# Kernel optimization log

Measured on AMD Instinct MI355X. Metric: run time of the kernel, lower is better.

## Reference

```python
import jax, jax.numpy as jnp
import numpy as np

C = 256          # channels
KS = 7           # kernel_size
G = 256          # groups (defaults to channels)
HID = C // 4     # hidden = channels // reduction
BN_EPS = 1e-5


def setup_inputs() -> dict:
    key = jax.random.key(0)
    ks = jax.random.split(key, 4)
    B, H, W = 4, 64, 64
    return {
        "x": jax.random.normal(ks[0], (B, C, H, W), jnp.float32),
        "reduce_w": jax.random.normal(ks[1], (HID, C), jnp.float32) / np.float32(np.sqrt(C)),
        "bn_gamma": jnp.ones((HID,), jnp.float32),
        "bn_beta": jnp.zeros((HID,), jnp.float32),
        "bn_mean": jnp.zeros((HID,), jnp.float32),
        "bn_var": jnp.ones((HID,), jnp.float32),
        "kproj_w": jax.random.normal(ks[2], (KS * KS * G, HID), jnp.float32) / np.float32(np.sqrt(HID)),
        "kproj_b": jnp.zeros((KS * KS * G,), jnp.float32),
    }


def _kernels(x, reduce_w, bn_gamma, bn_beta, bn_mean, bn_var, kproj_w, kproj_b):
    # 1x1 conv -> BN (eval mode) -> ReLU -> 1x1 conv, then per-pixel L2 kernel norm
    B, _, H, W = x.shape
    h = jnp.einsum('bchw,oc->bohw', x, reduce_w)
    inv = bn_gamma / jnp.sqrt(bn_var + BN_EPS)
    h = h * inv[None, :, None, None] + (bn_beta - bn_mean * inv)[None, :, None, None]
    h = jax.nn.relu(h)
    ker = jnp.einsum('bchw,oc->bohw', h, kproj_w) + kproj_b[None, :, None, None]
    ker = ker.reshape(B, G, KS * KS, H, W)           # (B, G, k*k, H, W)
    # kernel_norm == 'l2': zero-mean + unit L2 norm over the k*k taps
    ker = ker - ker.mean(axis=2, keepdims=True)
    denom = jnp.maximum(jnp.sqrt(jnp.sum(ker * ker, axis=2, keepdims=True)), 1e-6)
    return ker / denom


def reference(x, reduce_w, bn_gamma, bn_beta, bn_mean, bn_var, kproj_w, kproj_b):
    # get_kernels is under @torch.no_grad() in the original -> stop_gradient
    ker = jax.lax.stop_gradient(
        _kernels(x, reduce_w, bn_gamma, bn_beta, bn_mean, bn_var, kproj_w, kproj_b))
    B, Cc, H, W = x.shape
    pad = KS // 2
    gc = Cc // G  # = 1 for depthwise involution
    xp = jnp.pad(x, ((0, 0), (0, 0), (pad, pad), (pad, pad)))
    xg = xp.reshape(B, G, gc, H + 2 * pad, W + 2 * pad)
    # fused unfold-multiply-accumulate over the k*k taps (no (B,C,k,k,H,W) tensor)
    out = jnp.zeros((B, G, gc, H, W), x.dtype)
    for t in range(KS * KS):
        i, j = divmod(t, KS)
        out = out + xg[:, :, :, i:i + H, j:j + W] * ker[:, :, t][:, :, None]
    return out.reshape(B, Cc, H, W)
```

## Files before the change

### kernel.cpp

```cpp
#include <hip/hip_runtime.h>


#define C_    256
#define HID_  64
#define KS_   7
#define KK_   49
#define G_    256
#define H_    64
#define W_    64
#define HW_   4096
#define BN_EPS 1e-5f

typedef __attribute__((ext_vector_type(8)))  short bf16x8;
typedef __attribute__((ext_vector_type(4)))  float f32x4;
typedef __attribute__((ext_vector_type(16))) float f32x16;
typedef __attribute__((ext_vector_type(2)))  unsigned uv2;

__device__ __forceinline__ ushort f2bf(float f) {
    unsigned u = __float_as_uint(f);
    return (ushort)((u + 0x7fffu + ((u >> 16) & 1u)) >> 16);
}
__device__ __forceinline__ float bf2f(ushort s) {
    return __uint_as_float((unsigned)s << 16);
}
__device__ __forceinline__ float xor32p(float v) {
#if __has_builtin(__builtin_amdgcn_permlane32_swap)
    uv2 r = __builtin_amdgcn_permlane32_swap(__float_as_uint(v), __float_as_uint(v),
                                             false, false);
    return (__uint_as_float(r[0]) + __uint_as_float(r[1])) - v;
#else
    return __shfl_xor(v, 32);
#endif
}

__global__ __launch_bounds__(256) void prep_kernel(
    const float* __restrict__ kw, const float* __restrict__ kb,
    const float* __restrict__ reduce_w,
    const float* __restrict__ bn_gamma, const float* __restrict__ bn_beta,
    const float* __restrict__ bn_mean, const float* __restrict__ bn_var,
    ushort* __restrict__ kwb, float* __restrict__ rwT, float* __restrict__ betp,
    float* __restrict__ kbp)
{
    const int bid = blockIdx.x;
    if (bid < 256) {
        int idx  = bid * 256 + threadIdx.x;
        int base = idx * 16;
        int g    = base >> 12;
        int rem  = base & 4095;
        int tp   = rem >> 6;
        int k0   = rem & 63;
        if (tp >= 56) return;
        union { ushort s[16]; uint4 v[2]; } u;
        if ((tp & 7) < 7) {
            int t = (tp >> 3) * 7 + (tp & 7);
            const float* src = kw + ((size_t)(g * KK_ + t)) * HID_ + k0;
            #pragma unroll
            for (int i = 0; i < 16; ++i) u.s[i] = f2bf(src[i]);
        } else {
            #pragma unroll
            for (int i = 0; i < 16; ++i) u.s[i] = 0;
        }
        uint4* dst = (uint4*)(kwb + base);
        dst[0] = u.v[0];
        dst[1] = u.v[1];
    } else if (bid == 256) {
        int k = threadIdx.x;
        #pragma unroll 1
        for (int o = 0; o < HID_; ++o) {
            float inv = bn_gamma[o] * rsqrtf(bn_var[o] + BN_EPS);
            rwT[k * HID_ + o] = reduce_w[o * C_ + k] * inv;
        }
        if (k < HID_) {
            float inv = bn_gamma[k] * rsqrtf(bn_var[k] + BN_EPS);
            betp[k] = bn_beta[k] - bn_mean[k] * inv;
        }
    } else if (bid == 257) {
        for (int i = threadIdx.x; i < G_ * 64; i += 256) {
            int g = i >> 6, tp = i & 63;
            if (tp >= 56) continue;
            kbp[i] = ((tp & 7) < 7) ? kb[g * KK_ + (tp >> 3) * 7 + (tp & 7)] : 0.f;
        }
    } else {
        const int g = bid - 258;
        __shared__ float part[4][64];
        const int k  = threadIdx.x & 63;
        const int pr = threadIdx.x >> 6;
        const int t0 = pr * 13;
        const int t1 = (t0 + 13 < KK_) ? t0 + 13 : KK_;
        float s = 0.f;
        for (int t = t0; t < t1; ++t)
            s += kw[((size_t)(g * KK_ + t)) * HID_ + k];
        part[pr][k] = s;
        __syncthreads();
        if (threadIdx.x < 64) {
            float u = part[0][k] + part[1][k] + part[2][k] + part[3][k];
            ushort uh = f2bf(u);
            ushort ul = f2bf(u - bf2f(uh));
            ushort* kg = kwb + (size_t)g * 4096;
            kg[56 * 64 + k] = uh;  kg[60 * 64 + k] = uh;
            kg[57 * 64 + k] = ul;  kg[61 * 64 + k] = ul;
            kg[58 * 64 + k] = 0;   kg[59 * 64 + k] = 0;
            kg[62 * 64 + k] = 0;   kg[63 * 64 + k] = 0;
            float bs = (k < KK_) ? kb[g * KK_ + k] : 0.f;
            #pragma unroll
            for (int off = 32; off >= 1; off >>= 1) bs += __shfl_xor(bs, off);
            if (k == 0) {
                float* bg = kbp + g * 64;
                bg[56] = bs; bg[60] = bs;
                bg[57] = 0.f; bg[58] = 0.f; bg[59] = 0.f;
                bg[61] = 0.f; bg[62] = 0.f; bg[63] = 0.f;
            }
        }
    }
}

__global__ __launch_bounds__(256) void hv1_kernel(
    const float* __restrict__ x, const float* __restrict__ rwT,
    float* __restrict__ hvp, int npx)
{
    const int lane = threadIdx.x & 63;
    const int wq   = __builtin_amdgcn_readfirstlane(threadIdx.x >> 6);
    const int kq   = blockIdx.y;
    const int p    = blockIdx.x * 64 + lane;
    const int b    = p >> 12;
    const int hw   = p & 4095;

    float acc[16];
    #pragma unroll
    for (int j = 0; j < 16; ++j) acc[j] = 0.f;

    const float* xp = x + ((size_t)b * C_ + kq * 64) * HW_ + hw;
    const float* rw = rwT + (kq * 64) * HID_ + wq * 16;
    #pragma unroll 8
    for (int kk = 0; kk < 64; ++kk) {
        float xk = xp[(size_t)kk * HW_];
        #pragma unroll
        for (int j = 0; j < 16; ++j) acc[j] = fmaf(xk, rw[kk * HID_ + j], acc[j]);
    }
    float* dst = hvp + ((size_t)(kq * 64 + wq * 16)) * npx + p;
    #pragma unroll
    for (int j = 0; j < 16; ++j) dst[(size_t)j * npx] = acc[j];
}

__global__ __launch_bounds__(256) void hv2_kernel(
    const float* __restrict__ hvp, const float* __restrict__ betp,
    ushort* __restrict__ hv, int npx)
{
    const int p  = blockIdx.x * 256 + threadIdx.x;
    const int o0 = blockIdx.y * 4;
    ushort s[4];
    #pragma unroll
    for (int j = 0; j < 4; ++j) {
        float v = 0.f;
        #pragma unroll
        for (int kq = 0; kq < 4; ++kq)
            v += hvp[(size_t)(kq * 64 + o0 + j) * npx + p];
        s[j] = f2bf(fmaxf(v + betp[o0 + j], 0.f));
    }
    uint2 w;
    w.x = (uint)s[0] | ((uint)s[1] << 16);
    w.y = (uint)s[2] | ((uint)s[3] << 16);
    *(uint2*)(hv + (size_t)p * HID_ + o0) = w;
}

__global__ __launch_bounds__(256) void hv_kernel(
    const float* __restrict__ x, const float* __restrict__ rwT,
    const float* __restrict__ betp, ushort* __restrict__ hv)
{
    const int lane = threadIdx.x & 63;
    const int q    = __builtin_amdgcn_readfirstlane(threadIdx.x >> 6);
    const int p    = blockIdx.x * 64 + lane;
    const int b    = p >> 12;
    const int hw   = p & 4095;
    float acc[16];
    #pragma unroll
    for (int j = 0; j < 16; ++j) acc[j] = betp[q * 16 + j];
    const float* xp = x + (size_t)b * C_ * HW_ + hw;
    #pragma unroll 8
    for (int k = 0; k < C_; ++k) {
        float xk = xp[(size_t)k * HW_];
        const float* rw = rwT + k * HID_ + q * 16;
        #pragma unroll
        for (int j = 0; j < 16; ++j) acc[j] = fmaf(xk, rw[j], acc[j]);
    }
    union { ushort s[16]; uint4 v[2]; } u;
    #pragma unroll
    for (int j = 0; j < 16; ++j) u.s[j] = f2bf(fmaxf(acc[j], 0.f));
    uint4* dst = (uint4*)(hv + (size_t)p * HID_ + q * 16);
    dst[0] = u.v[0];
    dst[1] = u.v[1];
}

__global__ __launch_bounds__(64) void invol_main(
    const float* __restrict__ x, const ushort* __restrict__ hv,
    const ushort* __restrict__ kwb, const float* __restrict__ kbp,
    float* __restrict__ out)
{
    __shared__ float x_s[22][72];
    __shared__ float hs_s[22][64];

    const int lane = threadIdx.x;
    const int bg   = blockIdx.x;
    const int b    = bg >> 8;
    const int g    = bg & 255;
    const int y0   = blockIdx.y << 4;
    const int l31  = lane & 31;
    const int h4   = (lane >> 5) * 4;
    const int kl16 = (lane >> 5) * 16;
    const int c0   = h4 + l31;

    const float* xg = x + (size_t)bg * HW_;
    for (int idx = lane; idx < 22 * 72; idx += 64) {
        int r = idx / 72, c = idx - r * 72;
        int yy = y0 - 3 + r;
        int cc = c - 3;
        bool v = ((unsigned)yy < 64u) && ((unsigned)cc < 64u);
        x_s[r][c] = v ? xg[yy * 64 + cc] : 0.f;
    }

    bf16x8 ka[2][4];
    const char* kwg = (const char*)kwb + (size_t)g * 8192;
    #pragma unroll
    for (int m = 0; m < 2; ++m)
        #pragma unroll
        for (int s = 0; s < 4; ++s)
            ka[m][s] = *(const bf16x8*)(kwg + (m * 32 + l31) * 128 + s * 32 + kl16);
    const float* kbg = kbp + g * 64 + h4;

    __syncthreads();

    for (int t = lane; t < 88; t += 64) {
        int r   = t >> 2;
        int cc0 = (t & 3) << 4;
        float v[22];
        #pragma unroll
        for (int i = 0; i < 22; ++i) v[i] = x_s[r][cc0 + i];
        float s = v[0] + v[1] + v[2] + v[3] + v[4] + v[5] + v[6];
        hs_s[r][cc0] = s;
        #pragma unroll
        for (int c = 1; c < 16; ++c) {
            s += v[c + 6] - v[c - 1];
            hs_s[r][cc0 + c] = s;
        }
    }
    __syncthreads();

    const int rowpix0 = (b << 12) + (y0 << 6);

    #pragma unroll 2
    for (int ry = 0; ry < 16; ++ry) {
        bf16x8 hb0[4], hb1[4];
        const char* hvrow = (const char*)hv + (size_t)(rowpix0 + (ry << 6)) * 128;
        #pragma unroll
        for (int s = 0; s < 4; ++s) {
            hb0[s] = *(const bf16x8*)(hvrow + l31 * 128 + s * 32 + kl16);
            hb1[s] = *(const bf16x8*)(hvrow + (32 + l31) * 128 + s * 32 + kl16);
        }
        f32x4 kv0[4], kv1[4];
        #pragma unroll
        for (int q = 0; q < 4; ++q) {
            kv0[q] = *(const f32x4*)(kbg + q * 8);
            kv1[q] = *(const f32x4*)(kbg + 32 + q * 8);
        }

        float x2 = hs_s[ry][lane] + hs_s[ry + 1][lane] + hs_s[ry + 2][lane]
                 + hs_s[ry + 3][lane] + hs_s[ry + 4][lane]
                 + hs_s[ry + 5][lane] + hs_s[ry + 6][lane];

        f32x16 acc00, acc01, acc10, acc11;
        #pragma unroll
        for (int q = 0; q < 4; ++q)
            #pragma unroll
            for (int e = 0; e < 4; ++e) {
                acc00[q * 4 + e] = kv0[q][e];
                acc01[q * 4 + e] = kv0[q][e];
                acc10[q * 4 + e] = kv1[q][e];
                acc11[q * 4 + e] = kv1[q][e];
            }
        #pragma unroll
        for (int s = 0; s < 4; ++s) {
            acc00 = __builtin_amdgcn_mfma_f32_32x32x16_bf16(ka[0][s], hb0[s], acc00, 0, 0, 0);
            acc01 = __builtin_amdgcn_mfma_f32_32x32x16_bf16(ka[0][s], hb1[s], acc01, 0, 0, 0);
            acc10 = __builtin_amdgcn_mfma_f32_32x32x16_bf16(ka[1][s], hb0[s], acc10, 0, 0, 0);
            acc11 = __builtin_amdgcn_mfma_f32_32x32x16_bf16(ka[1][s], hb1[s], acc11, 0, 0, 0);
        }

        float ssq0 = 0.f, ssq1 = 0.f;
        #pragma unroll
        for (int r = 0; r < 16; ++r) {
            ssq0 = fmaf(acc00[r], acc00[r], ssq0);
            ssq1 = fmaf(acc01[r], acc01[r], ssq1);
        }
        #pragma unroll
        for (int r = 0; r < 12; ++r) {
            ssq0 = fmaf(acc10[r], acc10[r], ssq0);
            ssq1 = fmaf(acc11[r], acc11[r], ssq1);
        }
        float mn0 = (acc10[12] + acc10[13]) * (1.f / 49.f);
        float mn1 = (acc11[12] + acc11[13]) * (1.f / 49.f);

        float kx0 = 0.f, kx1 = 0.f;
        const float* xb = &x_s[ry][0];
        #pragma unroll
        for (int q = 0; q < 4; ++q) {
            const float* bp = xb + q * 72 + c0;
            #pragma unroll
            for (int e = 0; e < 4; ++e) {
                kx0 = fmaf(acc00[q * 4 + e], bp[e], kx0);
                kx1 = fmaf(acc01[q * 4 + e], bp[32 + e], kx1);
            }
        }
        #pragma unroll
        for (int q = 0; q < 3; ++q) {
            const float* bp = xb + (4 + q) * 72 + c0;
            #pragma unroll
            for (int e = 0; e < 4; ++e) {
                kx0 = fmaf(acc10[q * 4 + e], bp[e], kx0);
                kx1 = fmaf(acc11[q * 4 + e], bp[32 + e], kx1);
            }
        }

        const bool lo = lane < 32;
        float kx_own = lo ? kx0 : kx1, kx_cr = lo ? kx1 : kx0;
        float ss_own = lo ? ssq0 : ssq1, ss_cr = lo ? ssq1 : ssq0;
        float mo     = lo ? mn0 : mn1;
        float kxo = kx_own + xor32p(kx_cr);
        float sso = ss_own + xor32p(ss_cr);

        float ss = fmaxf(sso - 49.f * mo * mo, 0.f);
        float is = 1.f / fmaxf(sqrtf(ss), 1e-6f);
        out[(size_t)bg * HW_ + ((y0 + ry) << 6) + lane] = (kxo - mo * x2) * is;
    }
}

__global__ __launch_bounds__(256) void invol_fallback(
    const float* __restrict__ x, const float* __restrict__ reduce_w,
    const float* __restrict__ bn_gamma, const float* __restrict__ bn_beta,
    const float* __restrict__ bn_mean, const float* __restrict__ bn_var,
    const float* __restrict__ kw, const float* __restrict__ kb,
    float* __restrict__ out)
{
    __shared__ float rwT[C_][HID_ + 4];
    __shared__ float bns[HID_];
    __shared__ float bnb[HID_];
    const int tid = threadIdx.x;
    const int b  = blockIdx.z;
    const int g0 = blockIdx.y * 32;
    const int p  = blockIdx.x * 256 + tid;
    const int py = p >> 6;
    const int px = p & 63;
    #pragma unroll 1
    for (int o = 0; o < HID_; ++o) rwT[tid][o] = reduce_w[o * C_ + tid];
    if (tid < HID_) {
        float inv = bn_gamma[tid] * rsqrtf(bn_var[tid] + BN_EPS);
        bns[tid] = inv;
        bnb[tid] = bn_beta[tid] - bn_mean[tid] * inv;
    }
    __syncthreads();
    float hvv[HID_];
    #pragma unroll
    for (int o = 0; o < HID_; ++o) hvv[o] = 0.f;
    const float* xb = x + (size_t)b * C_ * HW_ + p;
    #pragma unroll 4
    for (int k = 0; k < C_; ++k) {
        float xk = xb[(size_t)k * HW_];
        const float4* wr = (const float4*)&rwT[k][0];
        #pragma unroll
        for (int o4 = 0; o4 < HID_ / 4; ++o4) {
            float4 w = wr[o4];
            hvv[o4*4+0] = fmaf(xk, w.x, hvv[o4*4+0]);
            hvv[o4*4+1] = fmaf(xk, w.y, hvv[o4*4+1]);
            hvv[o4*4+2] = fmaf(xk, w.z, hvv[o4*4+2]);
            hvv[o4*4+3] = fmaf(xk, w.w, hvv[o4*4+3]);
        }
    }
    #pragma unroll
    for (int o = 0; o < HID_; ++o) hvv[o] = fmaxf(fmaf(hvv[o], bns[o], bnb[o]), 0.f);
    #pragma unroll 1
    for (int gi = 0; gi < 32; ++gi) {
        const int g = g0 + gi;
        const float* kwg = kw + (size_t)g * KK_ * HID_;
        float acc[KK_];
        #pragma unroll
        for (int t = 0; t < KK_; ++t) {
            float a = kb[g * KK_ + t];
            const float4* row = (const float4*)(kwg + t * HID_);
            #pragma unroll
            for (int k4 = 0; k4 < HID_ / 4; ++k4) {
                float4 w = row[k4];
                a = fmaf(w.x, hvv[k4*4+0], a);
                a = fmaf(w.y, hvv[k4*4+1], a);
                a = fmaf(w.z, hvv[k4*4+2], a);
                a = fmaf(w.w, hvv[k4*4+3], a);
            }
            acc[t] = a;
        }
        float mean = 0.f;
        #pragma unroll
        for (int t = 0; t < KK_; ++t) mean += acc[t];
        mean *= (1.f / 49.f);
        float ss = 0.f;
        #pragma unroll
        for (int t = 0; t < KK_; ++t) { acc[t] -= mean; ss = fmaf(acc[t], acc[t], ss); }
        float inv = 1.f / fmaxf(sqrtf(ss), 1e-6f);
        const float* xg = x + ((size_t)(b * G_ + g)) * HW_;
        float oacc = 0.f;
        #pragma unroll
        for (int i = 0; i < KS_; ++i) {
            int yv = py + i - 3;
            bool rok = ((unsigned)yv < (unsigned)H_);
            const float* xrow = xg + yv * W_;
            #pragma unroll
            for (int j = 0; j < KS_; ++j) {
                int xx = px + j - 3;
                bool ok = rok && ((unsigned)xx < (unsigned)W_);
                float v = ok ? xrow[xx] : 0.f;
                oacc = fmaf(v, acc[i*7+j], oacc);
            }
        }
        out[((size_t)(b * G_ + g)) * HW_ + p] = oacc * inv;
    }
}

extern "C" void kernel_launch(void* const* d_in, const int* in_sizes, int n_in,
                              void* d_out, int out_size, void* d_ws, size_t ws_size,
                              hipStream_t stream) {
    const float* x        = (const float*)d_in[0];
    const float* reduce_w = (const float*)d_in[1];
    const float* bn_gamma = (const float*)d_in[2];
    const float* bn_beta  = (const float*)d_in[3];
    const float* bn_mean  = (const float*)d_in[4];
    const float* bn_var   = (const float*)d_in[5];
    const float* kproj_w  = (const float*)d_in[6];
    const float* kproj_b  = (const float*)d_in[7];
    float* out = (float*)d_out;
    const int B   = in_sizes[0] / (C_ * HW_);
    const int npx = B * HW_;

    size_t kwb_off = 0;
    size_t kwb_sz  = (size_t)G_ * 64 * 64 * 2;
    size_t kbp_off = kwb_off + kwb_sz;
    size_t kbp_sz  = (size_t)G_ * 64 * 4;
    size_t rwt_off = kbp_off + kbp_sz;
    size_t rwt_sz  = (size_t)C_ * HID_ * 4;
    size_t bet_off = rwt_off + rwt_sz;
    size_t bet_sz  = 256;
    size_t hv_off  = bet_off + bet_sz;
    size_t hv_sz   = (size_t)npx * HID_ * 2;
    size_t hvp_off = hv_off + hv_sz;
    size_t hvp_sz  = (size_t)4 * HID_ * npx * 4;
    size_t need2   = hvp_off;
    size_t need    = hvp_off + hvp_sz;

    if (ws_size < need2) {
        dim3 grid(HW_ / 256, G_ / 32, B);
        invol_fallback<<<grid, 256, 0, stream>>>(x, reduce_w, bn_gamma, bn_beta,
                                                 bn_mean, bn_var, kproj_w, kproj_b, out);
        return;
    }

    ushort* kwb  = (ushort*)((char*)d_ws + kwb_off);
    float*  kbp  = (float*)((char*)d_ws + kbp_off);
    float*  rwT  = (float*)((char*)d_ws + rwt_off);
    float*  betp = (float*)((char*)d_ws + bet_off);
    ushort* hv   = (ushort*)((char*)d_ws + hv_off);
    float*  hvp  = (float*)((char*)d_ws + hvp_off);

    prep_kernel<<<dim3(258 + G_), 256, 0, stream>>>(kproj_w, kproj_b, reduce_w,
                                                    bn_gamma, bn_beta, bn_mean, bn_var,
                                                    kwb, rwT, betp, kbp);
    if (ws_size >= need) {
        hv1_kernel<<<dim3(npx / 64, 4), 256, 0, stream>>>(x, rwT, hvp, npx);
        hv2_kernel<<<dim3(npx / 256, 16), 256, 0, stream>>>(hvp, betp, hv, npx);
    } else {
        hv_kernel<<<dim3(npx / 64), 256, 0, stream>>>(x, rwT, betp, hv);
    }
    invol_main<<<dim3(B * G_, 4), 64, 0, stream>>>(x, hv, kwb, kbp, out);
}
```

Before: 124.8 us.

## Halve row tile per block, split MFMA halves sequentially, slide vertical box sum

Each invol_main block now covers 8 output rows instead of 16, so the grid doubles to 8 blocks per (batch, group). The per-row work processes the two 32-pixel halves one after another with two accumulators instead of four, which lowers register pressure and should raise occupancy. The vertical 7-row box sum x2 is now updated incrementally instead of recomputed every row. In exchange, the halo rows of x and the kernel weight loads are repeated across twice as many blocks, and the extra xor shuffles per half add some cost.

```diff
diff --git a/kernel.cpp b/kernel.cpp
--- a/kernel.cpp
+++ b/kernel.cpp
@@ -196,21 +196,21 @@
     const ushort* __restrict__ kwb, const float* __restrict__ kbp,
     float* __restrict__ out)
 {
-    __shared__ float x_s[22][72];
-    __shared__ float hs_s[22][64];
+    __shared__ float x_s[14][72];
+    __shared__ float hs_s[14][64];
 
     const int lane = threadIdx.x;
     const int bg   = blockIdx.x;
     const int b    = bg >> 8;
     const int g    = bg & 255;
-    const int y0   = blockIdx.y << 4;
+    const int y0   = blockIdx.y << 3;
     const int l31  = lane & 31;
     const int h4   = (lane >> 5) * 4;
     const int kl16 = (lane >> 5) * 16;
     const int c0   = h4 + l31;
 
     const float* xg = x + (size_t)bg * HW_;
-    for (int idx = lane; idx < 22 * 72; idx += 64) {
+    for (int idx = lane; idx < 14 * 72; idx += 64) {
         int r = idx / 72, c = idx - r * 72;
         int yy = y0 - 3 + r;
         int cc = c - 3;
@@ -229,9 +229,9 @@
 
     __syncthreads();
 
-    for (int t = lane; t < 88; t += 64) {
-        int r   = t >> 2;
-        int cc0 = (t & 3) << 4;
+    if (lane < 56) {
+        int r   = lane >> 2;
+        int cc0 = (lane & 3) << 4;
         float v[22];
         #pragma unroll
         for (int i = 0; i < 22; ++i) v[i] = x_s[r][cc0 + i];
@@ -247,89 +247,75 @@
 
     const int rowpix0 = (b << 12) + (y0 << 6);
 
+    float x2 = hs_s[0][lane] + hs_s[1][lane] + hs_s[2][lane] + hs_s[3][lane]
+             + hs_s[4][lane] + hs_s[5][lane] + hs_s[6][lane];
+
     #pragma unroll 2
-    for (int ry = 0; ry < 16; ++ry) {
-        bf16x8 hb0[4], hb1[4];
+    for (int ry = 0; ry < 8; ++ry) {
         const char* hvrow = (const char*)hv + (size_t)(rowpix0 + (ry << 6)) * 128;
-        #pragma unroll
-        for (int s = 0; s < 4; ++s) {
-            hb0[s] = *(const bf16x8*)(hvrow + l31 * 128 + s * 32 + kl16);
-            hb1[s] = *(const bf16x8*)(hvrow + (32 + l31) * 128 + s * 32 + kl16);
-        }
         f32x4 kv0[4], kv1[4];
         #pragma unroll
         for (int q = 0; q < 4; ++q) {
             kv0[q] = *(const f32x4*)(kbg + q * 8);
             kv1[q] = *(const f32x4*)(kbg + 32 + q * 8);
         }
-
-        float x2 = hs_s[ry][lane] + hs_s[ry + 1][lane] + hs_s[ry + 2][lane]
-                 + hs_s[ry + 3][lane] + hs_s[ry + 4][lane]
-                 + hs_s[ry + 5][lane] + hs_s[ry + 6][lane];
-
-        f32x16 acc00, acc01, acc10, acc11;
-        #pragma unroll
-        for (int q = 0; q < 4; ++q)
-            #pragma unroll
-            for (int e = 0; e < 4; ++e) {
-                acc00[q * 4 + e] = kv0[q][e];
-                acc01[q * 4 + e] = kv0[q][e];
-                acc10[q * 4 + e] = kv1[q][e];
-                acc11[q * 4 + e] = kv1[q][e];
-            }
-        #pragma unroll
-        for (int s = 0; s < 4; ++s) {
-            acc00 = __builtin_amdgcn_mfma_f32_32x32x16_bf16(ka[0][s], hb0[s], acc00, 0, 0, 0);
-            acc01 = __builtin_amdgcn_mfma_f32_32x32x16_bf16(ka[0][s], hb1[s], acc01, 0, 0, 0);
-            acc10 = __builtin_amdgcn_mfma_f32_32x32x16_bf16(ka[1][s], hb0[s], acc10, 0, 0, 0);
-            acc11 = __builtin_amdgcn_mfma_f32_32x32x16_bf16(ka[1][s], hb1[s], acc11, 0, 0, 0);
-        }
-
-        float ssq0 = 0.f, ssq1 = 0.f;
-        #pragma unroll
-        for (int r = 0; r < 16; ++r) {
-            ssq0 = fmaf(acc00[r], acc00[r], ssq0);
-            ssq1 = fmaf(acc01[r], acc01[r], ssq1);
-        }
-        #pragma unroll
-        for (int r = 0; r < 12; ++r) {
-            ssq0 = fmaf(acc10[r], acc10[r], ssq0);
-            ssq1 = fmaf(acc11[r], acc11[r], ssq1);
-        }
-        float mn0 = (acc10[12] + acc10[13]) * (1.f / 49.f);
-        float mn1 = (acc11[12] + acc11[13]) * (1.f / 49.f);
-
-        float kx0 = 0.f, kx1 = 0.f;
         const float* xb = &x_s[ry][0];
-        #pragma unroll
-        for (int q = 0; q < 4; ++q) {
-            const float* bp = xb + q * 72 + c0;
-            #pragma unroll
-            for (int e = 0; e < 4; ++e) {
-                kx0 = fmaf(acc00[q * 4 + e], bp[e], kx0);
-                kx1 = fmaf(acc01[q * 4 + e], bp[32 + e], kx1);
-            }
-        }
-        #pragma unroll
-        for (int q = 0; q < 3; ++q) {
-            const float* bp = xb + (4 + q) * 72 + c0;
-            #pragma unroll
-            for (int e = 0; e < 4; ++e) {
-                kx0 = fmaf(acc10[q * 4 + e], bp[e], kx0);
-                kx1 = fmaf(acc11[q * 4 + e], bp[32 + e], kx1);
-            }
-        }
-
-        const bool lo = lane < 32;
-        float kx_own = lo ? kx0 : kx1, kx_cr = lo ? kx1 : kx0;
-        float ss_own = lo ? ssq0 : ssq1, ss_cr = lo ? ssq1 : ssq0;
-        float mo     = lo ? mn0 : mn1;
-        float kxo = kx_own + xor32p(kx_cr);
-        float sso = ss_own + xor32p(ss_cr);
-
-        float ss = fmaxf(sso - 49.f * mo * mo, 0.f);
-        float is = 1.f / fmaxf(sqrtf(ss), 1e-6f);
-        out[(size_t)bg * HW_ + ((y0 + ry) << 6) + lane] = (kxo - mo * x2) * is;
+
+        float ov[2];
+        #pragma unroll
+        for (int nh = 0; nh < 2; ++nh) {
+            bf16x8 hb[4];
+            #pragma unroll
+            for (int s = 0; s < 4; ++s)
+                hb[s] = *(const bf16x8*)(hvrow + (nh * 32 + l31) * 128 + s * 32 + kl16);
+
+            f32x16 acc0, acc1;
+            #pragma unroll
+            for (int q = 0; q < 4; ++q)
+                #pragma unroll
+                for (int e = 0; e < 4; ++e) {
+                    acc0[q * 4 + e] = kv0[q][e];
+                    acc1[q * 4 + e] = kv1[q][e];
+                }
+            #pragma unroll
+            for (int s = 0; s < 4; ++s) {
+                acc0 = __builtin_amdgcn_mfma_f32_32x32x16_bf16(ka[0][s], hb[s], acc0, 0, 0, 0);
+                acc1 = __builtin_amdgcn_mfma_f32_32x32x16_bf16(ka[1][s], hb[s], acc1, 0, 0, 0);
+            }
+
+            float ssq = 0.f;
+            #pragma unroll
+            for (int r = 0; r < 16; ++r) ssq = fmaf(acc0[r], acc0[r], ssq);
+            #pragma unroll
+            for (int r = 0; r < 12; ++r) ssq = fmaf(acc1[r], acc1[r], ssq);
+            float mo = (acc1[12] + acc1[13]) * (1.f / 49.f);
+
+            float kx = 0.f;
+            const int cb = c0 + nh * 32;
+            #pragma unroll
+            for (int q = 0; q < 4; ++q) {
+                const float* bp = xb + q * 72 + cb;
+                #pragma unroll
+                for (int e = 0; e < 4; ++e) kx = fmaf(acc0[q * 4 + e], bp[e], kx);
+            }
+            #pragma unroll
+            for (int q = 0; q < 3; ++q) {
+                const float* bp = xb + (4 + q) * 72 + cb;
+                #pragma unroll
+                for (int e = 0; e < 4; ++e) kx = fmaf(acc1[q * 4 + e], bp[e], kx);
+            }
+
+            float kxo = kx + xor32p(kx);
+            float sso = ssq + xor32p(ssq);
+            float ss  = fmaxf(sso - 49.f * mo * mo, 0.f);
+            float is  = 1.f / fmaxf(sqrtf(ss), 1e-6f);
+            ov[nh] = (kxo - mo * x2) * is;
+        }
+
+        float outv = (lane < 32) ? ov[0] : ov[1];
+        out[(size_t)bg * HW_ + ((y0 + ry) << 6) + lane] = outv;
+
+        if (ry < 7) x2 += hs_s[ry + 7][lane] - hs_s[ry][lane];
     }
 }
 
@@ -475,5 +461,5 @@
     } else {
         hv_kernel<<<dim3(npx / 64), 256, 0, stream>>>(x, rwT, betp, hv);
     }
-    invol_main<<<dim3(B * G_, 4), 64, 0, stream>>>(x, hv, kwb, kbp, out);
-}
+    invol_main<<<dim3(B * G_, 8), 64, 0, stream>>>(x, hv, kwb, kbp, out);
+}
```

After: 129.6 us. 3.8% more time.
